# Kernel tuning notes

Measured on AMD Instinct MI355X. Metric: run time of the kernel, lower is better.

The kernel has to match this reference:

```python
import jax, jax.numpy as jnp
import numpy as np

B, T, V, D, H = 256, 64, 6207, 512, 512  # batch, seq_len, vocab, emb_dim, hidden_dim
YF = 2048   # image feature dim -> concat with h (512) = 2560 gate input
EPS = 1e-10


def setup_inputs() -> dict:
    key = jax.random.key(0)
    ks = jax.random.split(key, 20)
    # torch init_parameters(): all params ~ U(-0.05, 0.05)
    u = lambda k, s: jax.random.uniform(k, s, jnp.float32, -0.05, 0.05)
    return {
        "y": jax.random.normal(ks[0], (B, YF), jnp.float32),
        "x": jax.random.randint(ks[1], (B, T), 0, V),
        "emb_w": u(ks[2], (V, D)),
        # bottom LSTM cell (input 512 -> hidden 512), torch layout: W_ih (4H, D)
        "W_ih": u(ks[3], (4 * H, D)), "W_hh": u(ks[4], (4 * H, H)),
        "b_ih": u(ks[5], (4 * H,)), "b_hh": u(ks[6], (4 * H,)),
        # top LSTM cell (input 512 -> hidden 512)
        "W_ih_t": u(ks[7], (4 * H, H)), "W_hh_t": u(ks[8], (4 * H, H)),
        "b_ih_t": u(ks[9], (4 * H,)), "b_hh_t": u(ks[10], (4 * H,)),
        # gate linear: Linear(2560, 512)
        "Wg": u(ks[11], (H, H + YF)), "bg": u(ks[12], (H,)),
        # final linear: Linear(512, 256)
        "Wlin": u(ks[13], (256, H)), "blin": u(ks[14], (256,)),
        # per-step gumbel-sigmoid uniforms (sampled inside forward in torch;
        # precomputed here so the reference is deterministic)
        "u1": jax.random.uniform(ks[15], (T, B, H), jnp.float32),
        "u2": jax.random.uniform(ks[16], (T, B, H), jnp.float32),
    }


def _lstm_cell(xt, h, c, Wi, Wh, bi, bh):
    # torch nn.LSTM gate order: i, f, g, o
    z = xt @ Wi.T + bi + h @ Wh.T + bh          # (B, 4H)
    i, f, g, o = jnp.split(z, 4, axis=-1)
    c = jax.nn.sigmoid(f) * c + jax.nn.sigmoid(i) * jnp.tanh(g)
    h = jax.nn.sigmoid(o) * jnp.tanh(c)
    return h, c


def reference(y, x, emb_w, W_ih, W_hh, b_ih, b_hh,
              W_ih_t, W_hh_t, b_ih_t, b_hh_t, Wg, bg, Wlin, blin, u1, u2):
    xs = jnp.transpose(emb_w[x], (1, 0, 2))     # (T, B, D)

    def step(carry, ins):
        h, c, ht, ct = carry
        xt, u1t, u2t = ins
        h, c = _lstm_cell(xt, h, c, W_ih, W_hh, b_ih, b_hh)
        # gate logits: relu(Linear([h, y]))
        logits = jax.nn.relu(jnp.concatenate([h, y], axis=1) @ Wg.T + bg)
        # custom gumbel-sigmoid noise: -log(log(U2+eps)/log(U1+eps)+eps)
        noise = -jnp.log(jnp.log(u2t + EPS) / jnp.log(u1t + EPS) + EPS)
        y_soft = jax.nn.sigmoid(logits + noise)
        # hard threshold at 0.5 with straight-through estimator
        y_hard = (y_soft >= 0.5).astype(y_soft.dtype)
        gate = y_hard - jax.lax.stop_gradient(y_soft) + y_soft
        hf = h * gate
        ht, ct = _lstm_cell(hf, ht, ct, W_ih_t, W_hh_t, b_ih_t, b_hh_t)
        return (h, c, ht, ct), None

    z0 = jnp.zeros((B, H), jnp.float32)
    (_, _, ht, _), _ = jax.lax.scan(step, (z0, z0, z0, z0), (xs, u1, u2))
    # dropout is identity in eval mode; torch output is (1, B, 256), squeezed here
    return jax.nn.relu(ht @ Wlin.T + blin)      # (B, 256)
```

## Files before the change

### kernel.cpp

```cpp
#include <hip/hip_runtime.h>
#include <hip/hip_bf16.h>


typedef __attribute__((ext_vector_type(8))) short short8;
typedef __attribute__((ext_vector_type(4))) float floatx4;
typedef __attribute__((ext_vector_type(4))) unsigned int uintx4;

#define MFMA16(a, b, c) __builtin_amdgcn_mfma_f32_16x16x32_bf16(a, b, c, 0, 0, 0)
#define AGENT __HIP_MEMORY_SCOPE_AGENT
#define HWREG_XCC_ID ((31u << 11) | (0u << 6) | 20u)

__device__ inline float bf2f(ushort u) {
    union { unsigned int u32; float f; } v; v.u32 = ((unsigned int)u) << 16; return v.f;
}
__device__ inline ushort f2bf(float f) {
    union { float f; unsigned int u; } v; v.f = f;
    return (ushort)((v.u + 0x7fffu + ((v.u >> 16) & 1u)) >> 16);
}
__device__ inline short8 ld8(const ushort* p) { return *(const short8*)p; }
__device__ inline float sigf(float x) { return 1.0f / (1.0f + expf(-x)); }
__device__ inline void mm3(floatx4& acc, short8 ah, short8 al, short8 bh, short8 bl) {
    acc = MFMA16(ah, bh, acc);
    acc = MFMA16(ah, bl, acc);
    acc = MFMA16(al, bh, acc);
}

__global__ __launch_bounds__(256) void k_prep(const float* __restrict__ w0,
                                              const float* __restrict__ w1,
                                              const float* __restrict__ w2,
                                              const float* __restrict__ w3,
                                              const float* __restrict__ wg,
                                              const float* __restrict__ wl,
                                              const float* __restrict__ em,
                                              const float* __restrict__ yy,
                                              ushort* __restrict__ wreg,
                                              uint* __restrict__ zbase) {
    unsigned i = blockIdx.x * 256u + threadIdx.x;
    if (i >= 9866784u) return;
    if (i >= 9338368u) {
        zbase[i - 9338368u] = 0u;
        return;
    }
    const float* src; ushort* hi; unsigned n, loc;
    if (i < 4194304u) {
        unsigned seg = i >> 20; loc = i & 1048575u; n = 1048576u;
        hi = wreg + seg * 2097152u;
        src = (seg == 0) ? w0 : (seg == 1) ? w1 : (seg == 2) ? w2 : w3;
    } else if (i < 5505024u) { loc = i - 4194304u; src = wg; hi = wreg + 8388608u;  n = 1310720u; }
    else if (i < 5636096u)   { loc = i - 5505024u; src = wl; hi = wreg + 11010048u; n = 131072u; }
    else if (i < 8814080u)   { loc = i - 5636096u; src = em; hi = wreg + 11272192u; n = 3177984u; }
    else                     { loc = i - 8814080u; src = yy; hi = wreg + 17628160u; n = 524288u; }
    float v = src[loc];
    ushort h = f2bf(v);
    hi[loc] = h;
    hi[n + loc] = f2bf(v - bf2f(h));
}

__global__ __launch_bounds__(512) void k_gy(const ushort* __restrict__ y_hi,
                                            const ushort* __restrict__ y_lo,
                                            const ushort* __restrict__ Wg_hi,
                                            const ushort* __restrict__ Wg_lo,
                                            const float* __restrict__ bg,
                                            float* __restrict__ gy) {
    __shared__ float zsB[4 * 528];
    int tid = threadIdx.x, lane = tid & 63, w = tid >> 6;
    int quad = lane >> 4, lr = lane & 15, q8 = quad * 8;
    int r0 = (blockIdx.x >> 4) * 16, n0 = (blockIdx.x & 15) * 32;
    int nh = w & 1, kq = w >> 1;
    int arow = r0 + lr, brow = n0 + nh * 16 + lr;
    floatx4 acc = {};
#pragma unroll
    for (int k0 = 0; k0 < 512; k0 += 32) {
        short8 ah = ld8(y_hi + arow * 2048 + kq * 512 + k0 + q8);
        short8 al = ld8(y_lo + arow * 2048 + kq * 512 + k0 + q8);
        short8 bh = ld8(Wg_hi + brow * 2560 + 512 + kq * 512 + k0 + q8);
        short8 bl = ld8(Wg_lo + brow * 2560 + 512 + kq * 512 + k0 + q8);
        mm3(acc, ah, al, bh, bl);
    }
#pragma unroll
    for (int r4 = 0; r4 < 4; r4++)
        zsB[kq * 528 + (quad * 4 + r4) * 33 + nh * 16 + lr] = acc[r4];
    __syncthreads();
    int ml = tid >> 5, jj = tid & 31;
    float s = zsB[ml * 33 + jj] + zsB[528 + ml * 33 + jj] +
              zsB[1056 + ml * 33 + jj] + zsB[1584 + ml * 33 + jj];
    gy[(r0 + ml) * 512 + n0 + jj] = s + bg[n0 + jj];
}

struct KP {
    const float *b_ih, *b_hh, *b_iht, *b_hht, *u1, *u2, *gy;
    const int* x;
    uint *hseq, *bseq, *tseq;
    uint* claim;
    uint *hP0, *hP1, *htP0, *htP1, *bitsP;
    ushort *ht_hi, *ht_lo;
    const ushort *Whh_hi, *Whh_lo, *Wih_hi, *Wih_lo;
    const ushort *Wiht_hi, *Wiht_lo, *Whht_hi, *Whht_lo;
    const ushort *Wg_hi, *Wg_lo, *em_hi, *em_lo;
};

__device__ inline void publish(uint* sq, uint v) {
    asm volatile("" ::: "memory");
    __builtin_amdgcn_s_waitcnt(0);
    __syncthreads();
    if (threadIdx.x == 0)
        __hip_atomic_store(sq, v, __ATOMIC_RELAXED, AGENT);
}
__device__ inline void poll16(const uint* sq, uint target) {
    if ((threadIdx.x >> 6) == 0) {
        int l = threadIdx.x & 63;
        for (;;) {
            uint v = (l < 16) ? __hip_atomic_load(&sq[l], __ATOMIC_RELAXED, AGENT) : target;
            if (__all((int)(v >= target))) break;
            __builtin_amdgcn_s_sleep(1);
        }
    }
    __syncthreads();
}

__device__ inline void issue_row16(const uint* __restrict__ src, int r0, uintx4* v) {
    int tid = threadIdx.x;
    int sr = tid >> 5, scol = (tid & 31) * 16;
    const uint* pp = src + (r0 + sr) * 512 + scol;
    asm volatile(
        "global_load_dwordx4 %0, %4, off sc0 sc1\n\t"
        "global_load_dwordx4 %1, %4, off offset:16 sc0 sc1\n\t"
        "global_load_dwordx4 %2, %4, off offset:32 sc0 sc1\n\t"
        "global_load_dwordx4 %3, %4, off offset:48 sc0 sc1"
        : "=v"(v[0]), "=v"(v[1]), "=v"(v[2]), "=v"(v[3])
        : "v"(pp) : "memory");
}
__device__ inline void unpack_row16(const uintx4* v, ushort* __restrict__ dst) {
    int tid = threadIdx.x;
    int sr = tid >> 5, scol = (tid & 31) * 16;
    ushort* d = dst + sr * 1032 + scol;
    union { uint u[4]; short8 s; } H0, H1, L0, L1;
    H0.u[0] = (v[0][0] & 0xffffu) | (v[0][1] << 16);
    H0.u[1] = (v[0][2] & 0xffffu) | (v[0][3] << 16);
    H0.u[2] = (v[1][0] & 0xffffu) | (v[1][1] << 16);
    H0.u[3] = (v[1][2] & 0xffffu) | (v[1][3] << 16);
    L0.u[0] = (v[0][0] >> 16) | (v[0][1] & 0xffff0000u);
    L0.u[1] = (v[0][2] >> 16) | (v[0][3] & 0xffff0000u);
    L0.u[2] = (v[1][0] >> 16) | (v[1][1] & 0xffff0000u);
    L0.u[3] = (v[1][2] >> 16) | (v[1][3] & 0xffff0000u);
    H1.u[0] = (v[2][0] & 0xffffu) | (v[2][1] << 16);
    H1.u[1] = (v[2][2] & 0xffffu) | (v[2][3] << 16);
    H1.u[2] = (v[3][0] & 0xffffu) | (v[3][1] << 16);
    H1.u[3] = (v[3][2] & 0xffffu) | (v[3][3] << 16);
    L1.u[0] = (v[2][0] >> 16) | (v[2][1] & 0xffff0000u);
    L1.u[1] = (v[2][2] >> 16) | (v[2][3] & 0xffff0000u);
    L1.u[2] = (v[3][0] >> 16) | (v[3][1] & 0xffff0000u);
    L1.u[3] = (v[3][2] >> 16) | (v[3][3] & 0xffff0000u);
    *(short8*)(d) = H0.s;
    *(short8*)(d + 8) = H1.s;
    *(short8*)(d + 520) = L0.s;
    *(short8*)(d + 520 + 8) = L1.s;
}

__device__ inline void stage_emb(const ushort* __restrict__ emh,
                                 const ushort* __restrict__ eml,
                                 const int* __restrict__ x, int r0, int t,
                                 ushort* __restrict__ dst) {
    int tid = threadIdx.x;
    int sr = tid >> 5, sc = (tid & 31) * 16;
    int tok = x[(r0 + sr) * 64 + t];
    const short8* ph = (const short8*)(emh + (size_t)tok * 512 + sc);
    const short8* pl = (const short8*)(eml + (size_t)tok * 512 + sc);
    short8 h0 = ph[0], h1 = ph[1], l0 = pl[0], l1 = pl[1];
    ushort* d = dst + sr * 1032;
    *(short8*)(d + sc) = h0;       *(short8*)(d + sc + 8) = h1;
    *(short8*)(d + 520 + sc) = l0; *(short8*)(d + 520 + sc + 8) = l1;
}

__device__ inline short8 fragA(const ushort* As, int row, int k) {
    return *(const short8*)(As + row * 1032 + k);
}

__device__ inline void pub_state(const uint* __restrict__ hx, uint* __restrict__ dst,
                                 int r0, int j0, int lane) {
    const uintx4* s = (const uintx4*)(hx + lane * 8);
    uintx4 a = s[0], b = s[1];
    uint* d = dst + (r0 + (lane >> 2)) * 512 + j0 + ((lane * 8) & 31);
    asm volatile("global_store_dwordx4 %0, %1, off sc0 sc1\n\t"
                 "global_store_dwordx4 %0, %2, off offset:16 sc0 sc1"
                 :: "v"(d), "v"(a), "v"(b) : "memory");
}

__global__ void __launch_bounds__(512, 1) k_main(KP p) {
    __shared__ ushort As[16 * 1032];
    __shared__ ushort Ae[16 * 1032];
    __shared__ ushort Az[16 * 1032];
    __shared__ ushort Ac[16 * 1032];
    __shared__ float zsD[4224];
    __shared__ uint gbits[256];
    __shared__ uint hx[512];
    __shared__ uint role_s;

    const int tid = threadIdx.x;
    const int w = tid >> 6;
    const int lane = tid & 63;
    const int quad = lane >> 4;
    const int lr = lane & 15;
    const int q8 = quad * 8;
    const float EPS = 1e-10f;

    if (tid == 0) {
        uint xcc = __builtin_amdgcn_s_getreg(HWREG_XCC_ID) & 7u;
        uint slot = __hip_atomic_fetch_add(&p.claim[xcc * 16], 1u,
                                           __ATOMIC_RELAXED, AGENT) & 31u;
        role_s = xcc * 32u + slot;
    }
    __syncthreads();
    const uint role = role_s;
    const int jb = (int)(role >> 4);
    const int g16 = (int)(role & 15u);
    const int r0 = g16 * 16, j0 = jb * 32;

    const int g4 = w & 3, team = w >> 2;
    const int gate = w >> 1, nh = w & 1;
    const int brow = gate * 512 + j0 + nh * 16 + lr;
    const int kq = w >> 1;
    const int browB = j0 + nh * 16 + lr;
    const int ml = tid >> 5, jj = tid & 31;

    const float biasAe0 = p.b_ih[j0 + jj]        + p.b_hh[j0 + jj];
    const float biasAe1 = p.b_ih[512 + j0 + jj]  + p.b_hh[512 + j0 + jj];
    const float biasAe2 = p.b_ih[1024 + j0 + jj] + p.b_hh[1024 + j0 + jj];
    const float biasAe3 = p.b_ih[1536 + j0 + jj] + p.b_hh[1536 + j0 + jj];
    const float biasCe0 = p.b_iht[j0 + jj]        + p.b_hht[j0 + jj];
    const float biasCe1 = p.b_iht[512 + j0 + jj]  + p.b_hht[512 + j0 + jj];
    const float biasCe2 = p.b_iht[1024 + j0 + jj] + p.b_hht[1024 + j0 + jj];
    const float biasCe3 = p.b_iht[1536 + j0 + jj] + p.b_hht[1536 + j0 + jj];
    const float gy_r = p.gy[(r0 + ml) * 512 + j0 + jj];

    const int rowA = g4 * 512 + j0 + lr;
    const ushort* WAh = (team ? p.Wih_hi : p.Whh_hi) + rowA * 512;
    const ushort* WAl = (team ? p.Wih_lo : p.Whh_lo) + rowA * 512;
    const ushort* WitH = p.Wiht_hi + brow * 512;
    const ushort* WitL = p.Wiht_lo + brow * 512;
    const ushort* WgH = p.Wg_hi + browB * 2560 + kq * 128;
    const ushort* WgL = p.Wg_lo + browB * 2560 + kq * 128;
    const float* pu1 = p.u1 + (r0 + ml) * 512 + j0 + jj;
    const float* pu2 = p.u2 + (r0 + ml) * 512 + j0 + jj;
    uint* hs = p.hseq + g16 * 16;
    uint* bs = p.bseq + g16 * 16;
    uint* hts = p.tseq + g16 * 16;

    short8 wHt[16], wLt[16];
    {
        const ushort* WhtH = p.Whht_hi + brow * 512;
        const ushort* WhtL = p.Whht_lo + brow * 512;
#pragma unroll
        for (int kk = 0; kk < 16; kk++) {
            wHt[kk] = ld8(WhtH + kk * 32 + q8);
            wLt[kk] = ld8(WhtL + kk * 32 + q8);
        }
    }

    for (int i = tid; i < 16 * 1032; i += 512) As[i] = 0;
    stage_emb(p.em_hi, p.em_lo, p.x, r0, 0, Ae);
    float U1 = __builtin_nontemporal_load(pu1);
    float U2 = __builtin_nontemporal_load(pu2);
    __syncthreads();

    float c_reg = 0.0f, ct_reg = 0.0f;

    for (int t = 0; t < 64; t++) {
        {
            const ushort* Ax = team ? Ae : As;
            floatx4 acc0 = {}, acc1 = {};
#pragma unroll
            for (int k0 = 0; k0 < 512; k0 += 32) {
                short8 xh = fragA(Ax, lr, k0 + q8);
                short8 xl = fragA(Ax, lr, 520 + k0 + q8);
                mm3(acc0, xh, xl, ld8(WAh + k0 + q8), ld8(WAl + k0 + q8));
                mm3(acc1, xh, xl, ld8(WAh + 8192 + k0 + q8), ld8(WAl + 8192 + k0 + q8));
            }
#pragma unroll
            for (int r4 = 0; r4 < 4; r4++) {
                zsD[team * 2112 + (quad * 4 + r4) * 132 + g4 * 32 + lr]      = acc0[r4];
                zsD[team * 2112 + (quad * 4 + r4) * 132 + g4 * 32 + 16 + lr] = acc1[r4];
            }
        }
        if (t > 0) poll16(hts, (uint)t); else __syncthreads();
        uintx4 vz[4];
        issue_row16((t & 1) ? p.htP0 : p.htP1, r0, vz);
        uint* hPcur = (t & 1) ? p.hP1 : p.hP0;
        {
            float zi = (zsD[ml * 132 + jj]      + zsD[2112 + ml * 132 + jj])      + biasAe0;
            float zf = (zsD[ml * 132 + 32 + jj] + zsD[2112 + ml * 132 + 32 + jj]) + biasAe1;
            float zg = (zsD[ml * 132 + 64 + jj] + zsD[2112 + ml * 132 + 64 + jj]) + biasAe2;
            float zo = (zsD[ml * 132 + 96 + jj] + zsD[2112 + ml * 132 + 96 + jj]) + biasAe3;
            c_reg = sigf(zf) * c_reg + sigf(zi) * tanhf(zg);
            float hv = sigf(zo) * tanhf(c_reg);
            ushort hb = f2bf(hv);
            ushort lb = f2bf(hv - bf2f(hb));
            __hip_atomic_store(&hPcur[(r0 + ml) * 512 + j0 + jj],
                               (uint)hb | ((uint)lb << 16), __ATOMIC_RELAXED, AGENT);
        }
        asm volatile("s_waitcnt vmcnt(0)" ::: "memory");
        __builtin_amdgcn_sched_barrier(0);
        __syncthreads();
        if (tid == 0)
            __hip_atomic_store(&hs[jb], (uint)(t + 1), __ATOMIC_RELAXED, AGENT);
        unpack_row16(vz, Az);
        float noise = -logf(logf(U2 + EPS) / logf(U1 + EPS) + EPS);
        __syncthreads();
        floatx4 c2acc = {};
#pragma unroll
        for (int kk = 0; kk < 16; kk++)
            mm3(c2acc, fragA(Az, lr, kk * 32 + q8), fragA(Az, lr, 520 + kk * 32 + q8),
                wHt[kk], wLt[kk]);
#pragma unroll
        for (int r4 = 0; r4 < 4; r4++)
            zsD[2112 + (quad * 4 + r4) * 132 + gate * 32 + nh * 16 + lr] = c2acc[r4];
        poll16(hs, (uint)(t + 1));
        uintx4 va[4];
        issue_row16(hPcur, r0, va);
        asm volatile("s_waitcnt vmcnt(0)" ::: "memory");
        __builtin_amdgcn_sched_barrier(0);
        unpack_row16(va, As);
        __syncthreads();

        {
            floatx4 acc = {};
#pragma unroll
            for (int k0 = 0; k0 < 128; k0 += 32)
                mm3(acc, fragA(As, lr, kq * 128 + k0 + q8),
                    fragA(As, lr, 520 + kq * 128 + k0 + q8),
                    ld8(WgH + k0 + q8), ld8(WgL + k0 + q8));
#pragma unroll
            for (int r4 = 0; r4 < 4; r4++)
                zsD[kq * 528 + (quad * 4 + r4) * 33 + nh * 16 + lr] = acc[r4];
        }
        __syncthreads();
        {
            float z2 = zsD[ml * 33 + jj] + zsD[528 + ml * 33 + jj] +
                       zsD[1056 + ml * 33 + jj] + zsD[1584 + ml * 33 + jj];
            float logit = fmaxf(z2 + gy_r, 0.0f);
            bool gbit = sigf(logit + noise) >= 0.5f;
            unsigned long long bm = __ballot((int)gbit);
            if ((lane & 31) == 0)
                __hip_atomic_store(&p.bitsP[(r0 + ml) * 16 + jb],
                                   (uint)(bm >> ((lane >> 5) * 32)),
                                   __ATOMIC_RELAXED, AGENT);
        }
        publish(&bs[jb], (uint)(t + 1));
        if (t < 63) stage_emb(p.em_hi, p.em_lo, p.x, r0, t + 1, Ae);
        poll16(bs, (uint)(t + 1));
        uint rb = 0;
        if (tid < 256)
            asm volatile("global_load_dword %0, %1, off sc0 sc1"
                         : "=v"(rb) : "v"(p.bitsP + r0 * 16 + tid) : "memory");
        if (t < 63) {
            U1 = __builtin_nontemporal_load(pu1 + (t + 1) * 131072);
            U2 = __builtin_nontemporal_load(pu2 + (t + 1) * 131072);
            asm volatile("s_waitcnt vmcnt(2)" ::: "memory");
        } else {
            asm volatile("s_waitcnt vmcnt(0)" ::: "memory");
        }
        __builtin_amdgcn_sched_barrier(0);
        if (tid < 256) gbits[tid] = rb;
        __syncthreads();
        {
            int sr = tid >> 5, sc = (tid & 31) * 16;
            uint word = gbits[sr * 16 + (sc >> 5)];
            uint chunk = (word >> (sc & 16)) & 0xffffu;
            const ushort* as0 = As + sr * 1032 + sc;
            ushort* ac0 = Ac + sr * 1032 + sc;
            union { uint u[4]; short8 s; } m0, m1;
#pragma unroll
            for (int j = 0; j < 4; j++) {
                uint b0 = 0u - ((chunk >> (2 * j)) & 1u);
                uint b1 = 0u - ((chunk >> (2 * j + 1)) & 1u);
                m0.u[j] = (b0 & 0xffffu) | (b1 << 16);
            }
#pragma unroll
            for (int j = 0; j < 4; j++) {
                uint b0 = 0u - ((chunk >> (8 + 2 * j)) & 1u);
                uint b1 = 0u - ((chunk >> (8 + 2 * j + 1)) & 1u);
                m1.u[j] = (b0 & 0xffffu) | (b1 << 16);
            }
            short8 h0 = *(const short8*)(as0);
            short8 h1 = *(const short8*)(as0 + 8);
            short8 l0 = *(const short8*)(as0 + 520);
            short8 l1 = *(const short8*)(as0 + 528);
            *(short8*)(ac0)       = h0 & m0.s;
            *(short8*)(ac0 + 8)   = h1 & m1.s;
            *(short8*)(ac0 + 520) = l0 & m0.s;
            *(short8*)(ac0 + 528) = l1 & m1.s;
        }
        __syncthreads();
        {
            floatx4 c1acc = {};
#pragma unroll
            for (int k0 = 0; k0 < 512; k0 += 32)
                mm3(c1acc, fragA(Ac, lr, k0 + q8), fragA(Ac, lr, 520 + k0 + q8),
                    ld8(WitH + k0 + q8), ld8(WitL + k0 + q8));
#pragma unroll
            for (int r4 = 0; r4 < 4; r4++)
                zsD[(quad * 4 + r4) * 132 + gate * 32 + nh * 16 + lr] = c1acc[r4];
        }
        __syncthreads();
        {
            float zi = (zsD[ml * 132 + jj]      + zsD[2112 + ml * 132 + jj])      + biasCe0;
            float zf = (zsD[ml * 132 + 32 + jj] + zsD[2112 + ml * 132 + 32 + jj]) + biasCe1;
            float zg = (zsD[ml * 132 + 64 + jj] + zsD[2112 + ml * 132 + 64 + jj]) + biasCe2;
            float zo = (zsD[ml * 132 + 96 + jj] + zsD[2112 + ml * 132 + 96 + jj]) + biasCe3;
            ct_reg = sigf(zf) * ct_reg + sigf(zi) * tanhf(zg);
            float hv = sigf(zo) * tanhf(ct_reg);
            ushort hb = f2bf(hv);
            ushort lb = f2bf(hv - bf2f(hb));
            hx[ml * 32 + jj] = (uint)hb | ((uint)lb << 16);
            if (t == 63) {
                int idx = (r0 + ml) * 512 + j0 + jj;
                p.ht_hi[idx] = hb; p.ht_lo[idx] = lb;
            }
        }
        __syncthreads();
        if (w == 0) {
            uint* htcur = (t & 1) ? p.htP1 : p.htP0;
            pub_state(hx, htcur, r0, j0, lane);
            asm volatile("s_waitcnt vmcnt(0)" ::: "memory");
            if (lane == 0)
                __hip_atomic_store(&hts[jb], (uint)(t + 1), __ATOMIC_RELAXED, AGENT);
        }
    }
}

__global__ __launch_bounds__(256) void k_final(const ushort* __restrict__ ht_hi,
                                               const ushort* __restrict__ ht_lo,
                                               const ushort* __restrict__ Wl_hi,
                                               const ushort* __restrict__ Wl_lo,
                                               const float* __restrict__ blin,
                                               float* __restrict__ out) {
    int tid = threadIdx.x, lane = tid & 63, w = tid >> 6;
    int wm = w & 1, wn = w >> 1, quad = lane >> 4, lr = lane & 15;
    int m0 = blockIdx.y * 64, n0 = blockIdx.x * 64;
    floatx4 acc[2][2] = {};
    for (int k0 = 0; k0 < 512; k0 += 32) {
        short8 ah[2], al[2], bh[2], bl[2];
#pragma unroll
        for (int tn = 0; tn < 2; tn++) {
            int n = n0 + wn * 32 + tn * 16 + lr;
            bh[tn] = ld8(Wl_hi + n * 512 + k0 + quad * 8);
            bl[tn] = ld8(Wl_lo + n * 512 + k0 + quad * 8);
        }
#pragma unroll
        for (int tm = 0; tm < 2; tm++) {
            int r = m0 + wm * 32 + tm * 16 + lr;
            ah[tm] = ld8(ht_hi + r * 512 + k0 + quad * 8);
            al[tm] = ld8(ht_lo + r * 512 + k0 + quad * 8);
        }
#pragma unroll
        for (int tm = 0; tm < 2; tm++)
#pragma unroll
            for (int tn = 0; tn < 2; tn++) mm3(acc[tm][tn], ah[tm], al[tm], bh[tn], bl[tn]);
    }
#pragma unroll
    for (int tm = 0; tm < 2; tm++)
#pragma unroll
        for (int tn = 0; tn < 2; tn++)
#pragma unroll
            for (int r4 = 0; r4 < 4; r4++) {
                int row = m0 + wm * 32 + tm * 16 + quad * 4 + r4;
                int n = n0 + wn * 32 + tn * 16 + lr;
                out[row * 256 + n] = fmaxf(acc[tm][tn][r4] + blin[n], 0.0f);
            }
}

extern "C" void kernel_launch(void* const* d_in, const int* in_sizes, int n_in,
                              void* d_out, int out_size, void* d_ws, size_t ws_size,
                              hipStream_t stream) {
    (void)in_sizes; (void)n_in; (void)out_size; (void)ws_size;
    const float* y      = (const float*)d_in[0];
    const int*   x      = (const int*)d_in[1];
    const float* emb    = (const float*)d_in[2];
    const float* W_ih   = (const float*)d_in[3];
    const float* W_hh   = (const float*)d_in[4];
    const float* b_ih   = (const float*)d_in[5];
    const float* b_hh   = (const float*)d_in[6];
    const float* W_iht  = (const float*)d_in[7];
    const float* W_hht  = (const float*)d_in[8];
    const float* b_iht  = (const float*)d_in[9];
    const float* b_hht  = (const float*)d_in[10];
    const float* Wg     = (const float*)d_in[11];
    const float* bg     = (const float*)d_in[12];
    const float* Wlin   = (const float*)d_in[13];
    const float* blin   = (const float*)d_in[14];
    const float* u1     = (const float*)d_in[15];
    const float* u2     = (const float*)d_in[16];
    float* out = (float*)d_out;

    uint* bar  = (uint*)d_ws;
    uint* hP0  = bar + 4128;
    uint* hP1  = hP0 + 131072;
    uint* htP0 = hP1 + 131072;
    uint* htP1 = htP0 + 131072;
    float* gy  = (float*)(htP1 + 131072);
    ushort* ht_hi = (ushort*)(gy + 131072);
    ushort* ht_lo = ht_hi + 131072;
    uint* bitsP = (uint*)(ht_lo + 131072);
    ushort* wreg = (ushort*)(bitsP + 4096);

    KP p;
    p.b_ih = b_ih; p.b_hh = b_hh; p.b_iht = b_iht; p.b_hht = b_hht;
    p.u1 = u1; p.u2 = u2; p.gy = gy; p.x = x;
    p.hseq = bar; p.bseq = bar + 256; p.tseq = bar + 512; p.claim = bar + 1024;
    p.hP0 = hP0; p.hP1 = hP1; p.htP0 = htP0; p.htP1 = htP1; p.bitsP = bitsP;
    p.ht_hi = ht_hi; p.ht_lo = ht_lo;
    p.Wih_hi  = wreg;             p.Wih_lo  = wreg + 1048576;
    p.Whh_hi  = wreg + 2097152;   p.Whh_lo  = wreg + 3145728;
    p.Wiht_hi = wreg + 4194304;   p.Wiht_lo = wreg + 5242880;
    p.Whht_hi = wreg + 6291456;   p.Whht_lo = wreg + 7340032;
    p.Wg_hi   = wreg + 8388608;   p.Wg_lo   = wreg + 9699328;
    p.em_hi   = wreg + 11272192;  p.em_lo   = wreg + 14450176;
    const ushort* Wl_hi = wreg + 11010048; const ushort* Wl_lo = wreg + 11141120;
    const ushort* y_hi  = wreg + 17628160; const ushort* y_lo  = wreg + 18152448;

    k_prep<<<dim3(38543), dim3(256), 0, stream>>>(W_ih, W_hh, W_iht, W_hht, Wg, Wlin,
                                                  emb, y, wreg, bar);
    k_gy<<<dim3(256), dim3(512), 0, stream>>>(y_hi, y_lo, p.Wg_hi, p.Wg_lo, bg, gy);

    void* args[] = {(void*)&p};
    hipLaunchCooperativeKernel((const void*)k_main, dim3(256), dim3(512), args, 0, stream);

    k_final<<<dim3(4, 4), dim3(256), 0, stream>>>(ht_hi, ht_lo, Wl_hi, Wl_lo, blin, out);
}
```

Baseline: 2.256 ms.

## Software-pipeline top LSTM cell one step behind bottom cell to cut sync rounds

Restructures the per-step schedule so the top LSTM cell for step t-1 is computed alongside the bottom cell of step t. Both global state exchanges (h and ht) now share one combined poll. The masked copy into a separate LDS buffer is replaced by applying gate bitmasks directly to A fragments. The Wh_t product is moved after the gate publish to overlap the barrier wait, and a final epilogue finishes the last top step. This removes one cross-block synchronization round per step and several block barriers, at the cost of more complex dependency tracking and extra per-fragment mask work inside the MFMA loop.

Result: slower. 2.308 ms (+2.3%).

```diff
diff --git a/kernel.cpp b/kernel.cpp
--- a/kernel.cpp
+++ b/kernel.cpp
@@ -112,6 +112,20 @@
         for (;;) {
             uint v = (l < 16) ? __hip_atomic_load(&sq[l], __ATOMIC_RELAXED, AGENT) : target;
             if (__all((int)(v >= target))) break;
+            __builtin_amdgcn_s_sleep(1);
+        }
+    }
+    __syncthreads();
+}
+__device__ inline void poll_ht(const uint* hsq, const uint* tsq, uint th, uint tt) {
+    if ((threadIdx.x >> 6) == 0) {
+        int l = threadIdx.x & 63;
+        for (;;) {
+            uint v, tgt;
+            if (l < 16)      { v = __hip_atomic_load(&hsq[l], __ATOMIC_RELAXED, AGENT); tgt = th; }
+            else if (l < 32) { v = __hip_atomic_load(&tsq[l - 16], __ATOMIC_RELAXED, AGENT); tgt = tt; }
+            else             { v = 0u; tgt = 0u; }
+            if (__all((int)(v >= tgt))) break;
             __builtin_amdgcn_s_sleep(1);
         }
     }
@@ -176,24 +190,25 @@
     return *(const short8*)(As + row * 1032 + k);
 }
 
-__device__ inline void pub_state(const uint* __restrict__ hx, uint* __restrict__ dst,
-                                 int r0, int j0, int lane) {
-    const uintx4* s = (const uintx4*)(hx + lane * 8);
-    uintx4 a = s[0], b = s[1];
-    uint* d = dst + (r0 + (lane >> 2)) * 512 + j0 + ((lane * 8) & 31);
-    asm volatile("global_store_dwordx4 %0, %1, off sc0 sc1\n\t"
-                 "global_store_dwordx4 %0, %2, off offset:16 sc0 sc1"
-                 :: "v"(d), "v"(a), "v"(b) : "memory");
+__device__ inline short8 mask8(uint ch) {
+    union { uint u[4]; short8 s; } mk;
+#pragma unroll
+    for (int j = 0; j < 4; j++) {
+        uint b0 = 0u - ((ch >> (2 * j)) & 1u);
+        uint b1 = 0u - ((ch >> (2 * j + 1)) & 1u);
+        mk.u[j] = (b0 & 0xffffu) | (b1 << 16);
+    }
+    return mk.s;
 }
 
 __global__ void __launch_bounds__(512, 1) k_main(KP p) {
     __shared__ ushort As[16 * 1032];
     __shared__ ushort Ae[16 * 1032];
     __shared__ ushort Az[16 * 1032];
-    __shared__ ushort Ac[16 * 1032];
-    __shared__ float zsD[4224];
-    __shared__ uint gbits[256];
-    __shared__ uint hx[512];
+    __shared__ float zsDA[4224];
+    __shared__ float zsC1[2112];
+    __shared__ float zsC2[2112];
+    __shared__ uint gbitsT[256];
     __shared__ uint role_s;
 
     const int tid = threadIdx.x;
@@ -278,19 +293,17 @@
             }
 #pragma unroll
             for (int r4 = 0; r4 < 4; r4++) {
-                zsD[team * 2112 + (quad * 4 + r4) * 132 + g4 * 32 + lr]      = acc0[r4];
-                zsD[team * 2112 + (quad * 4 + r4) * 132 + g4 * 32 + 16 + lr] = acc1[r4];
+                zsDA[team * 2112 + (quad * 4 + r4) * 132 + g4 * 32 + lr]      = acc0[r4];
+                zsDA[team * 2112 + (quad * 4 + r4) * 132 + g4 * 32 + 16 + lr] = acc1[r4];
             }
         }
-        if (t > 0) poll16(hts, (uint)t); else __syncthreads();
-        uintx4 vz[4];
-        issue_row16((t & 1) ? p.htP0 : p.htP1, r0, vz);
+        __syncthreads();
         uint* hPcur = (t & 1) ? p.hP1 : p.hP0;
         {
-            float zi = (zsD[ml * 132 + jj]      + zsD[2112 + ml * 132 + jj])      + biasAe0;
-            float zf = (zsD[ml * 132 + 32 + jj] + zsD[2112 + ml * 132 + 32 + jj]) + biasAe1;
-            float zg = (zsD[ml * 132 + 64 + jj] + zsD[2112 + ml * 132 + 64 + jj]) + biasAe2;
-            float zo = (zsD[ml * 132 + 96 + jj] + zsD[2112 + ml * 132 + 96 + jj]) + biasAe3;
+            float zi = (zsDA[ml * 132 + jj]      + zsDA[2112 + ml * 132 + jj])      + biasAe0;
+            float zf = (zsDA[ml * 132 + 32 + jj] + zsDA[2112 + ml * 132 + 32 + jj]) + biasAe1;
+            float zg = (zsDA[ml * 132 + 64 + jj] + zsDA[2112 + ml * 132 + 64 + jj]) + biasAe2;
+            float zo = (zsDA[ml * 132 + 96 + jj] + zsDA[2112 + ml * 132 + 96 + jj]) + biasAe3;
             c_reg = sigf(zf) * c_reg + sigf(zi) * tanhf(zg);
             float hv = sigf(zo) * tanhf(c_reg);
             ushort hb = f2bf(hv);
@@ -298,30 +311,51 @@
             __hip_atomic_store(&hPcur[(r0 + ml) * 512 + j0 + jj],
                                (uint)hb | ((uint)lb << 16), __ATOMIC_RELAXED, AGENT);
         }
+        if (t > 0) {
+            floatx4 c1acc = {};
+#pragma unroll
+            for (int kk = 0; kk < 16; kk++) {
+                uint word = gbitsT[kk * 16 + lr];
+                short8 mk = mask8((word >> q8) & 0xffu);
+                short8 ah = fragA(As, lr, kk * 32 + q8) & mk;
+                short8 al = fragA(As, lr, 520 + kk * 32 + q8) & mk;
+                mm3(c1acc, ah, al, ld8(WitH + kk * 32 + q8), ld8(WitL + kk * 32 + q8));
+            }
+#pragma unroll
+            for (int r4 = 0; r4 < 4; r4++)
+                zsC1[(quad * 4 + r4) * 132 + gate * 32 + nh * 16 + lr] = c1acc[r4];
+        }
+        __syncthreads();
+        if (t > 0) {
+            float zi = (zsC1[ml * 132 + jj]      + zsC2[ml * 132 + jj])      + biasCe0;
+            float zf = (zsC1[ml * 132 + 32 + jj] + zsC2[ml * 132 + 32 + jj]) + biasCe1;
+            float zg = (zsC1[ml * 132 + 64 + jj] + zsC2[ml * 132 + 64 + jj]) + biasCe2;
+            float zo = (zsC1[ml * 132 + 96 + jj] + zsC2[ml * 132 + 96 + jj]) + biasCe3;
+            ct_reg = sigf(zf) * ct_reg + sigf(zi) * tanhf(zg);
+            float hv = sigf(zo) * tanhf(ct_reg);
+            ushort hb = f2bf(hv);
+            ushort lb = f2bf(hv - bf2f(hb));
+            uint* htcur = (t & 1) ? p.htP0 : p.htP1;
+            __hip_atomic_store(&htcur[(r0 + ml) * 512 + j0 + jj],
+                               (uint)hb | ((uint)lb << 16), __ATOMIC_RELAXED, AGENT);
+        }
         asm volatile("s_waitcnt vmcnt(0)" ::: "memory");
         __builtin_amdgcn_sched_barrier(0);
         __syncthreads();
-        if (tid == 0)
+        if (tid == 0) {
             __hip_atomic_store(&hs[jb], (uint)(t + 1), __ATOMIC_RELAXED, AGENT);
-        unpack_row16(vz, Az);
+            __hip_atomic_store(&hts[jb], (uint)t, __ATOMIC_RELAXED, AGENT);
+        }
         float noise = -logf(logf(U2 + EPS) / logf(U1 + EPS) + EPS);
-        __syncthreads();
-        floatx4 c2acc = {};
-#pragma unroll
-        for (int kk = 0; kk < 16; kk++)
-            mm3(c2acc, fragA(Az, lr, kk * 32 + q8), fragA(Az, lr, 520 + kk * 32 + q8),
-                wHt[kk], wLt[kk]);
-#pragma unroll
-        for (int r4 = 0; r4 < 4; r4++)
-            zsD[2112 + (quad * 4 + r4) * 132 + gate * 32 + nh * 16 + lr] = c2acc[r4];
-        poll16(hs, (uint)(t + 1));
-        uintx4 va[4];
+        poll_ht(hs, hts, (uint)(t + 1), (uint)t);
+        uintx4 va[4], vz[4];
         issue_row16(hPcur, r0, va);
+        issue_row16((t & 1) ? p.htP0 : p.htP1, r0, vz);
         asm volatile("s_waitcnt vmcnt(0)" ::: "memory");
         __builtin_amdgcn_sched_barrier(0);
         unpack_row16(va, As);
+        unpack_row16(vz, Az);
         __syncthreads();
-
         {
             floatx4 acc = {};
 #pragma unroll
@@ -331,12 +365,12 @@
                     ld8(WgH + k0 + q8), ld8(WgL + k0 + q8));
 #pragma unroll
             for (int r4 = 0; r4 < 4; r4++)
-                zsD[kq * 528 + (quad * 4 + r4) * 33 + nh * 16 + lr] = acc[r4];
+                zsDA[kq * 528 + (quad * 4 + r4) * 33 + nh * 16 + lr] = acc[r4];
         }
         __syncthreads();
         {
-            float z2 = zsD[ml * 33 + jj] + zsD[528 + ml * 33 + jj] +
-                       zsD[1056 + ml * 33 + jj] + zsD[1584 + ml * 33 + jj];
+            float z2 = zsDA[ml * 33 + jj] + zsDA[528 + ml * 33 + jj] +
+                       zsDA[1056 + ml * 33 + jj] + zsDA[1584 + ml * 33 + jj];
             float logit = fmaxf(z2 + gy_r, 0.0f);
             bool gbit = sigf(logit + noise) >= 0.5f;
             unsigned long long bm = __ballot((int)gbit);
@@ -347,6 +381,16 @@
         }
         publish(&bs[jb], (uint)(t + 1));
         if (t < 63) stage_emb(p.em_hi, p.em_lo, p.x, r0, t + 1, Ae);
+        {
+            floatx4 c2acc = {};
+#pragma unroll
+            for (int kk = 0; kk < 16; kk++)
+                mm3(c2acc, fragA(Az, lr, kk * 32 + q8),
+                    fragA(Az, lr, 520 + kk * 32 + q8), wHt[kk], wLt[kk]);
+#pragma unroll
+            for (int r4 = 0; r4 < 4; r4++)
+                zsC2[(quad * 4 + r4) * 132 + gate * 32 + nh * 16 + lr] = c2acc[r4];
+        }
         poll16(bs, (uint)(t + 1));
         uint rb = 0;
         if (tid < 256)
@@ -360,71 +404,35 @@
             asm volatile("s_waitcnt vmcnt(0)" ::: "memory");
         }
         __builtin_amdgcn_sched_barrier(0);
-        if (tid < 256) gbits[tid] = rb;
+        if (tid < 256) gbitsT[(tid & 15) * 16 + (tid >> 4)] = rb;
         __syncthreads();
-        {
-            int sr = tid >> 5, sc = (tid & 31) * 16;
-            uint word = gbits[sr * 16 + (sc >> 5)];
-            uint chunk = (word >> (sc & 16)) & 0xffffu;
-            const ushort* as0 = As + sr * 1032 + sc;
-            ushort* ac0 = Ac + sr * 1032 + sc;
-            union { uint u[4]; short8 s; } m0, m1;
-#pragma unroll
-            for (int j = 0; j < 4; j++) {
-                uint b0 = 0u - ((chunk >> (2 * j)) & 1u);
-                uint b1 = 0u - ((chunk >> (2 * j + 1)) & 1u);
-                m0.u[j] = (b0 & 0xffffu) | (b1 << 16);
-            }
-#pragma unroll
-            for (int j = 0; j < 4; j++) {
-                uint b0 = 0u - ((chunk >> (8 + 2 * j)) & 1u);
-                uint b1 = 0u - ((chunk >> (8 + 2 * j + 1)) & 1u);
-                m1.u[j] = (b0 & 0xffffu) | (b1 << 16);
-            }
-            short8 h0 = *(const short8*)(as0);
-            short8 h1 = *(const short8*)(as0 + 8);
-            short8 l0 = *(const short8*)(as0 + 520);
-            short8 l1 = *(const short8*)(as0 + 528);
-            *(short8*)(ac0)       = h0 & m0.s;
-            *(short8*)(ac0 + 8)   = h1 & m1.s;
-            *(short8*)(ac0 + 520) = l0 & m0.s;
-            *(short8*)(ac0 + 528) = l1 & m1.s;
-        }
-        __syncthreads();
-        {
-            floatx4 c1acc = {};
-#pragma unroll
-            for (int k0 = 0; k0 < 512; k0 += 32)
-                mm3(c1acc, fragA(Ac, lr, k0 + q8), fragA(Ac, lr, 520 + k0 + q8),
-                    ld8(WitH + k0 + q8), ld8(WitL + k0 + q8));
-#pragma unroll
-            for (int r4 = 0; r4 < 4; r4++)
-                zsD[(quad * 4 + r4) * 132 + gate * 32 + nh * 16 + lr] = c1acc[r4];
-        }
-        __syncthreads();
-        {
-            float zi = (zsD[ml * 132 + jj]      + zsD[2112 + ml * 132 + jj])      + biasCe0;
-            float zf = (zsD[ml * 132 + 32 + jj] + zsD[2112 + ml * 132 + 32 + jj]) + biasCe1;
-            float zg = (zsD[ml * 132 + 64 + jj] + zsD[2112 + ml * 132 + 64 + jj]) + biasCe2;
-            float zo = (zsD[ml * 132 + 96 + jj] + zsD[2112 + ml * 132 + 96 + jj]) + biasCe3;
-            ct_reg = sigf(zf) * ct_reg + sigf(zi) * tanhf(zg);
-            float hv = sigf(zo) * tanhf(ct_reg);
-            ushort hb = f2bf(hv);
-            ushort lb = f2bf(hv - bf2f(hb));
-            hx[ml * 32 + jj] = (uint)hb | ((uint)lb << 16);
-            if (t == 63) {
-                int idx = (r0 + ml) * 512 + j0 + jj;
-                p.ht_hi[idx] = hb; p.ht_lo[idx] = lb;
-            }
-        }
-        __syncthreads();
-        if (w == 0) {
-            uint* htcur = (t & 1) ? p.htP1 : p.htP0;
-            pub_state(hx, htcur, r0, j0, lane);
-            asm volatile("s_waitcnt vmcnt(0)" ::: "memory");
-            if (lane == 0)
-                __hip_atomic_store(&hts[jb], (uint)(t + 1), __ATOMIC_RELAXED, AGENT);
-        }
+    }
+    {
+        floatx4 c1acc = {};
+#pragma unroll
+        for (int kk = 0; kk < 16; kk++) {
+            uint word = gbitsT[kk * 16 + lr];
+            short8 mk = mask8((word >> q8) & 0xffu);
+            short8 ah = fragA(As, lr, kk * 32 + q8) & mk;
+            short8 al = fragA(As, lr, 520 + kk * 32 + q8) & mk;
+            mm3(c1acc, ah, al, ld8(WitH + kk * 32 + q8), ld8(WitL + kk * 32 + q8));
+        }
+#pragma unroll
+        for (int r4 = 0; r4 < 4; r4++)
+            zsC1[(quad * 4 + r4) * 132 + gate * 32 + nh * 16 + lr] = c1acc[r4];
+    }
+    __syncthreads();
+    {
+        float zi = (zsC1[ml * 132 + jj]      + zsC2[ml * 132 + jj])      + biasCe0;
+        float zf = (zsC1[ml * 132 + 32 + jj] + zsC2[ml * 132 + 32 + jj]) + biasCe1;
+        float zg = (zsC1[ml * 132 + 64 + jj] + zsC2[ml * 132 + 64 + jj]) + biasCe2;
+        float zo = (zsC1[ml * 132 + 96 + jj] + zsC2[ml * 132 + 96 + jj]) + biasCe3;
+        ct_reg = sigf(zf) * ct_reg + sigf(zi) * tanhf(zg);
+        float hv = sigf(zo) * tanhf(ct_reg);
+        ushort hb = f2bf(hv);
+        ushort lb = f2bf(hv - bf2f(hb));
+        int idx = (r0 + ml) * 512 + j0 + jj;
+        p.ht_hi[idx] = hb; p.ht_lo[idx] = lb;
     }
 }
 
```
